# Performance work log

Hardware: AMD Instinct MI355X
Metric: run time of the kernel (lower is better)

The kernel has to match this reference:

```python
import jax, jax.numpy as jnp
import numpy as np

N_NODES = 100000
FEATURES, HIDDEN, CLASSES = 256, 128, 32
N_EDGES = 1600000


def setup_inputs() -> dict:
    key = jax.random.key(0)
    k1, k2, k3, k4, k5 = jax.random.split(key, 5)
    x = jax.random.normal(k1, (N_NODES, FEATURES), dtype=jnp.float32)
    edge_index = jax.random.randint(k2, (2, N_EDGES), 0, N_NODES, dtype=jnp.int64)
    # GCNConv: Linear(in, out, bias=False) + separate bias added after aggregation
    s1 = 1.0 / np.sqrt(FEATURES)
    s2 = 1.0 / np.sqrt(HIDDEN)
    W1 = jax.random.uniform(k3, (FEATURES, HIDDEN), jnp.float32, -s1, s1)
    b1 = jnp.zeros((HIDDEN,), jnp.float32)
    W2 = jax.random.uniform(k4, (HIDDEN, CLASSES), jnp.float32, -s2, s2)
    b2 = jnp.zeros((CLASSES,), jnp.float32)
    return {"x": x, "W1": W1, "b1": b1, "W2": W2, "b2": b2, "edge_index": edge_index}


def _gcn_conv(x, edge_index, W, b, n_nodes):
    # PyG GCNConv with add_self_loops=False: out = D^{-1/2} A D^{-1/2} (X W) + b
    src, dst = edge_index[0], edge_index[1]
    h = x @ W  # [N, out]
    deg = jax.ops.segment_sum(jnp.ones_like(dst, dtype=h.dtype), dst, num_segments=n_nodes)
    dinv = jnp.where(deg > 0, jax.lax.rsqrt(jnp.maximum(deg, 1e-12)), 0.0)
    norm = dinv[src] * dinv[dst]  # [E]
    msgs = h[src] * norm[:, None]  # [E, out] gather + scale
    out = jax.ops.segment_sum(msgs, dst, num_segments=n_nodes)  # scatter-add
    return out + b


def reference(x, W1, b1, W2, b2, edge_index):
    h = _gcn_conv(x, edge_index, W1, b1, N_NODES)
    h = jax.nn.relu(h)
    # F.dropout(training=self.training): eval mode -> identity
    h = _gcn_conv(h, edge_index, W2, b2, N_NODES)
    return jax.nn.log_softmax(h, axis=1)
```

## Files before the change

### kernel.cpp

```cpp
#include <hip/hip_runtime.h>

typedef unsigned short u16;
typedef unsigned int   u32;
typedef __attribute__((ext_vector_type(8))) short short8;
typedef __attribute__((ext_vector_type(4))) float f32x4;
typedef __attribute__((ext_vector_type(2))) float f32x2;

constexpr int BSH = 9;
constexpr int BSZ = 1 << BSH;

__device__ inline float bf2f(u32 bits16) {
    union { u32 u; float f; } c; c.u = bits16 << 16; return c.f;
}
__device__ inline u16 f2bf(float f) {
    union { float f; u32 u; } c; c.f = f;
    return (u16)((c.u + 0x8000u) >> 16);
}
__device__ inline f32x2 up2(u32 h) {
    union { u32 u[2]; f32x2 f; } c;
    c.u[0] = h << 16;
    c.u[1] = h & 0xffff0000u;
    return c.f;
}
__device__ inline int ld_edge(const void* eb, int f64, size_t idx) {
    return f64 ? (int)((const long long*)eb)[idx] : ((const int*)eb)[idx];
}
__device__ inline void gl16(const void* g, void* l) {
    __builtin_amdgcn_global_load_lds(
        (const __attribute__((address_space(1))) unsigned int*)g,
        (__attribute__((address_space(3))) unsigned int*)l, 16, 0, 0);
}

__global__ void detect_kernel(const u32* xw, const int* ebuf_int, int* flags,
                              int* bucket_rsv, int nb, int CAP) {
    __shared__ int cnt;
    if (threadIdx.x == 0) cnt = 0;
    __syncthreads();
    u32 w = xw[threadIdx.x];
    int e = (int)((w >> 7) & 0xffu);
    if (e >= 110 && e <= 145) atomicAdd(&cnt, 1);
    int ev = ebuf_int[2 * threadIdx.x + 1];
    unsigned long long any = __ballot(ev != 0);
    if ((int)threadIdx.x < nb) bucket_rsv[threadIdx.x] = threadIdx.x * CAP;
    __syncthreads();
    if (threadIdx.x == 0) {
        flags[0] = (cnt < 192) ? 1 : 0;
        flags[1] = 0;
        flags[2] = (any == 0ULL) ? 1 : 0;
    }
}

__global__ void bconv_kernel(const void* b1, const void* b2, const int* flags,
                             float* b1f, float* b2f, int HID, int CLS) {
    int i = blockIdx.x * 256 + threadIdx.x;
    int f = flags[0];
    if (i < HID) b1f[i] = f ? ((const float*)b1)[i] : bf2f(((const u16*)b1)[i]);
    if (i < CLS) b2f[i] = f ? ((const float*)b2)[i] : bf2f(((const u16*)b2)[i]);
}

__global__ __launch_bounds__(256)
void passA_kernel(const void* eb, const int* flags, int* bucket_rsv,
                  int2* bpair, int E, int nb, int CAP) {
    __shared__ int hist[256];
    __shared__ int rbase[256];
    hist[threadIdx.x] = 0;
    __syncthreads();
    int f64 = flags[2];
    int base = blockIdx.x * 8192;
    #pragma unroll
    for (int k = 0; k < 32; ++k) {
        int e = base + k * 256 + threadIdx.x;
        if (e < E) {
            int d = ld_edge(eb, f64, (size_t)E + e);
            atomicAdd(&hist[d >> BSH], 1);
        }
    }
    __syncthreads();
    {
        int b = threadIdx.x;
        int c = (b < nb) ? hist[b] : 0;
        rbase[b] = c ? atomicAdd(&bucket_rsv[b], c) : 0;
        hist[b] = 0;
    }
    __syncthreads();
    #pragma unroll
    for (int k = 0; k < 32; ++k) {
        int e = base + k * 256 + threadIdx.x;
        if (e < E) {
            int d = ld_edge(eb, f64, (size_t)E + e);
            int s = ld_edge(eb, f64, (size_t)e);
            int bb = d >> BSH;
            int r = atomicAdd(&hist[bb], 1);
            int pos = rbase[bb] + r;
            if (pos < (bb + 1) * CAP)
                bpair[pos] = make_int2(s, d);
        }
    }
}

__global__ void fillscan_kernel(const int* bucket_rsv, int* bucket_base,
                                int* row_start, int nb, int E, int N, int CAP) {
    __shared__ int wsum[4];
    int t = threadIdx.x, lane = t & 63, wv = t >> 6;
    int v = (t < nb) ? (bucket_rsv[t] - t * CAP) : 0;
    int inc = v;
    #pragma unroll
    for (int d = 1; d < 64; d <<= 1) {
        int tmp = __shfl_up(inc, d, 64);
        if (lane >= d) inc += tmp;
    }
    if (lane == 63) wsum[wv] = inc;
    __syncthreads();
    int off = 0;
    #pragma unroll
    for (int w = 0; w < 4; ++w) if (w < wv) off += wsum[w];
    int excl = off + inc - v;
    if (t <= nb) bucket_base[t] = (t == nb) ? E : excl;
    if (t == 0) row_start[N] = E;
}

__global__ __launch_bounds__(256)
void bucketF_kernel(const int2* __restrict__ bpair, const int* __restrict__ bucket_rsv,
                    const int* __restrict__ bucket_base, float* __restrict__ dinv,
                    int* __restrict__ row_start, int* __restrict__ csr, int N, int CAP) {
    __shared__ int lcnt[BSZ];
    __shared__ int lrow[BSZ];
    __shared__ int wsum[4];
    int b = blockIdx.x, d0 = b << BSH;
    int t = threadIdx.x, lane = t & 63, wv = t >> 6;
    lcnt[2 * t] = 0; lcnt[2 * t + 1] = 0;
    __syncthreads();
    int e0 = b * CAP;
    int e1 = bucket_rsv[b];
    for (int e = e0 + t; e < e1; e += 256)
        atomicAdd(&lcnt[bpair[e].y - d0], 1);
    __syncthreads();
    int c0 = lcnt[2 * t], c1 = lcnt[2 * t + 1];
    int p = c0 + c1;
    int inc = p;
    #pragma unroll
    for (int d = 1; d < 64; d <<= 1) {
        int tmp = __shfl_up(inc, d, 64);
        if (lane >= d) inc += tmp;
    }
    if (lane == 63) wsum[wv] = inc;
    __syncthreads();
    int off = 0;
    #pragma unroll
    for (int w = 0; w < 4; ++w) if (w < wv) off += wsum[w];
    int ex0 = off + inc - p;
    int bb = bucket_base[b];
    lrow[2 * t] = ex0;
    lrow[2 * t + 1] = ex0 + c0;
    int da = d0 + 2 * t, db = d0 + 2 * t + 1;
    if (da < N) { row_start[da] = bb + ex0;      dinv[da] = c0 ? rsqrtf((float)c0) : 0.f; }
    if (db < N) { row_start[db] = bb + ex0 + c0; dinv[db] = c1 ? rsqrtf((float)c1) : 0.f; }
    lcnt[2 * t] = 0; lcnt[2 * t + 1] = 0;
    __syncthreads();
    for (int e = e0 + t; e < e1; e += 256) {
        int2 pr = bpair[e];
        int li = pr.y - d0;
        int r = atomicAdd(&lcnt[li], 1);
        csr[bb + lrow[li] + r] = pr.x;
    }
}

template<int NT, int KT, int NCOLS>
__global__ void prepack_kernel(const void* W, const int* flags, u16* pack) {
    int p = blockIdx.x * 256 + threadIdx.x;
    constexpr int TOT = NT * KT * 64 * 8;
    if (p >= TOT) return;
    int j = p & 7, lane = (p >> 3) & 63, fk = p >> 9;
    int kk = fk % KT, nt = fk / KT;
    int n = nt * 16 + (lane & 15);
    int k = kk * 32 + (lane >> 4) * 8 + j;
    u16 v = flags[0] ? f2bf(((const float*)W)[k * NCOLS + n])
                     : ((const u16*)W)[k * NCOLS + n];
    pack[p] = v;
}

template<int NT, int NTF, int KT, int G>
__global__ __launch_bounds__(256)
void gemm1_kernel(const void* __restrict__ A, const int* __restrict__ ff,
                  const u16* __restrict__ Bpack, const float* __restrict__ dinv,
                  u16* __restrict__ C, int M) {
    constexpr int K = KT * 32;
    constexpr int Ncols = NTF * 16;
    constexpr int NSPLIT = NTF / NT;
    constexpr int BBYTES = NT * KT * 64 * 16;
    __shared__ short8 ldsB[NT * KT * 64];

    const int bh = blockIdx.x % NSPLIT;
    const int bm = blockIdx.x / NSPLIT;
    const int t = threadIdx.x;
    const int wave = t >> 6, lane = t & 63;

    {
        const char* gB = (const char*)Bpack + (size_t)bh * BBYTES;
        char* lB = (char*)ldsB;
        #pragma unroll
        for (int c = 0; c < BBYTES / 4096; ++c)
            gl16(gB + c * 4096 + t * 16, lB + c * 4096 + t * 16);
    }
    const bool fA = (*ff != 0);
    const int m0 = (bm * 4 + wave) * (16 * G);
    const int q = lane >> 4, l16 = lane & 15;

    int rowc[G];
    #pragma unroll
    for (int g = 0; g < G; ++g) {
        int r = m0 + g * 16 + l16;
        rowc[g] = (r < M) ? r : (M - 1);
    }

    f32x4 acc[G][NT];
    #pragma unroll
    for (int g = 0; g < G; ++g)
        #pragma unroll
        for (int nt = 0; nt < NT; ++nt) acc[g][nt] = (f32x4){0.f, 0.f, 0.f, 0.f};

    f32x4 raw[3][G][2];
    const float* Ap[G];
    if (fA) {
        #pragma unroll
        for (int g = 0; g < G; ++g)
            Ap[g] = (const float*)A + (size_t)rowc[g] * K + q * 8;
        #pragma unroll
        for (int pj = 0; pj < 2; ++pj)
            #pragma unroll
            for (int g = 0; g < G; ++g) {
                const float* p = Ap[g] + pj * 32;
                raw[pj][g][0] = ((const f32x4*)p)[0];
                raw[pj][g][1] = ((const f32x4*)p)[1];
            }
        __builtin_amdgcn_sched_barrier(0);
    }
    __syncthreads();

    if (fA) {
        #pragma unroll
        for (int kk = 0; kk < KT; ++kk) {
            if (kk + 2 < KT) {
                #pragma unroll
                for (int g = 0; g < G; ++g) {
                    const float* p = Ap[g] + (kk + 2) * 32;
                    raw[(kk + 2) % 3][g][0] = ((const f32x4*)p)[0];
                    raw[(kk + 2) % 3][g][1] = ((const f32x4*)p)[1];
                }
            }
            __builtin_amdgcn_sched_barrier(0);
            short8 a[G];
            #pragma unroll
            for (int g = 0; g < G; ++g) {
                f32x4 v0 = raw[kk % 3][g][0];
                f32x4 v1 = raw[kk % 3][g][1];
                union { short8 s; u16 u[8]; } pa;
                pa.u[0] = f2bf(v0[0]); pa.u[1] = f2bf(v0[1]);
                pa.u[2] = f2bf(v0[2]); pa.u[3] = f2bf(v0[3]);
                pa.u[4] = f2bf(v1[0]); pa.u[5] = f2bf(v1[1]);
                pa.u[6] = f2bf(v1[2]); pa.u[7] = f2bf(v1[3]);
                a[g] = pa.s;
            }
            #pragma unroll
            for (int nt = 0; nt < NT; ++nt) {
                short8 b = ldsB[(nt * KT + kk) * 64 + lane];
                #pragma unroll
                for (int g = 0; g < G; ++g)
                    acc[g][nt] = __builtin_amdgcn_mfma_f32_16x16x32_bf16(a[g], b, acc[g][nt], 0, 0, 0);
            }
        }
    } else {
        #pragma unroll
        for (int kk = 0; kk < KT; ++kk) {
            short8 a[G];
            #pragma unroll
            for (int g = 0; g < G; ++g)
                a[g] = ((const short8*)((const u16*)A + (size_t)rowc[g] * K))[kk * 4 + q];
            #pragma unroll
            for (int nt = 0; nt < NT; ++nt) {
                short8 b = ldsB[(nt * KT + kk) * 64 + lane];
                #pragma unroll
                for (int g = 0; g < G; ++g)
                    acc[g][nt] = __builtin_amdgcn_mfma_f32_16x16x32_bf16(a[g], b, acc[g][nt], 0, 0, 0);
            }
        }
    }

    #pragma unroll
    for (int g = 0; g < G; ++g) {
        float sc[4];
        #pragma unroll
        for (int r = 0; r < 4; ++r) {
            int rr = m0 + g * 16 + q * 4 + r;
            sc[r] = dinv[(rr < M) ? rr : (M - 1)];
        }
        #pragma unroll
        for (int nt = 0; nt < NT; ++nt) {
            int col = bh * (NT * 16) + nt * 16 + l16;
            #pragma unroll
            for (int r = 0; r < 4; ++r) {
                int rrow = m0 + g * 16 + q * 4 + r;
                if (rrow < M)
                    C[(size_t)rrow * Ncols + col] = f2bf(acc[g][nt][r] * sc[r]);
            }
        }
    }
}

template<int NT, int KT, int G>
__global__ __launch_bounds__(256)
void gemm_kernel(const void* __restrict__ A, const int* __restrict__ ff,
                 const u16* __restrict__ Bpack, const float* __restrict__ dinv,
                 u16* __restrict__ C, int M) {
    constexpr int K = KT * 32;
    constexpr int Ncols = NT * 16;
    __shared__ short8 lds[NT * KT * 64];
    for (int i = threadIdx.x; i < NT * KT * 64; i += 256)
        lds[i] = ((const short8*)Bpack)[i];
    bool fA = (*ff != 0);
    __syncthreads();
    int wave = threadIdx.x >> 6, lane = threadIdx.x & 63;
    int m0 = (blockIdx.x * 4 + wave) * (16 * G);
    if (m0 >= M) return;
    int q = lane >> 4;
    int rowc[G];
    #pragma unroll
    for (int g = 0; g < G; ++g) {
        int r = m0 + g * 16 + (lane & 15);
        rowc[g] = (r < M) ? r : (M - 1);
    }
    f32x4 acc[G][NT];
    #pragma unroll
    for (int g = 0; g < G; ++g)
        #pragma unroll
        for (int nt = 0; nt < NT; ++nt) acc[g][nt] = (f32x4){0.f, 0.f, 0.f, 0.f};
    #pragma unroll
    for (int kk = 0; kk < KT; ++kk) {
        short8 a[G];
        #pragma unroll
        for (int g = 0; g < G; ++g) {
            if (fA) {
                const float* Af = (const float*)A + (size_t)rowc[g] * K + kk * 32 + q * 8;
                f32x4 v0 = ((const f32x4*)Af)[0];
                f32x4 v1 = ((const f32x4*)Af)[1];
                union { short8 s; u16 u[8]; } pa;
                pa.u[0] = f2bf(v0[0]); pa.u[1] = f2bf(v0[1]);
                pa.u[2] = f2bf(v0[2]); pa.u[3] = f2bf(v0[3]);
                pa.u[4] = f2bf(v1[0]); pa.u[5] = f2bf(v1[1]);
                pa.u[6] = f2bf(v1[2]); pa.u[7] = f2bf(v1[3]);
                a[g] = pa.s;
            } else {
                a[g] = ((const short8*)((const u16*)A + (size_t)rowc[g] * K))[kk * 4 + q];
            }
        }
        #pragma unroll
        for (int nt = 0; nt < NT; ++nt) {
            short8 b = lds[(nt * KT + kk) * 64 + lane];
            #pragma unroll
            for (int g = 0; g < G; ++g)
                acc[g][nt] = __builtin_amdgcn_mfma_f32_16x16x32_bf16(a[g], b, acc[g][nt], 0, 0, 0);
        }
    }
    #pragma unroll
    for (int g = 0; g < G; ++g) {
        float sc[4];
        #pragma unroll
        for (int r = 0; r < 4; ++r) {
            int rr = m0 + g * 16 + q * 4 + r;
            sc[r] = dinv[(rr < M) ? rr : (M - 1)];
        }
        #pragma unroll
        for (int nt = 0; nt < NT; ++nt) {
            int col = nt * 16 + (lane & 15);
            #pragma unroll
            for (int r = 0; r < 4; ++r) {
                int rrow = m0 + g * 16 + q * 4 + r;
                if (rrow < M)
                    C[(size_t)rrow * Ncols + col] = f2bf(acc[g][nt][r] * sc[r]);
            }
        }
    }
}

__global__ __launch_bounds__(256)
void agg1_kernel(const u32* __restrict__ H32, const int* __restrict__ csr,
                 const int* __restrict__ row_start, const float* __restrict__ dinv,
                 const float* __restrict__ b1f, u32* __restrict__ H1, int N) {
    int wave = threadIdx.x >> 6, lane = threadIdx.x & 63;
    int n = blockIdx.x * 4 + wave;
    if (n >= N) return;
    int s0 = row_start[n], s1 = row_start[n + 1];
    f32x2 acc = {0.f, 0.f};
    for (int base = s0; base < s1; base += 64) {
        int m = s1 - base; if (m > 64) m = 64;
        int myidx = (lane < m) ? csr[base + lane] : 0;
        int j = 0;
        for (; j + 8 <= m; j += 8) {
            int i0 = __shfl(myidx, j);
            int i1 = __shfl(myidx, j + 1);
            int i2 = __shfl(myidx, j + 2);
            int i3 = __shfl(myidx, j + 3);
            int i4 = __shfl(myidx, j + 4);
            int i5 = __shfl(myidx, j + 5);
            int i6 = __shfl(myidx, j + 6);
            int i7 = __shfl(myidx, j + 7);
            u32 h0 = H32[(size_t)i0 * 64 + lane];
            u32 h1 = H32[(size_t)i1 * 64 + lane];
            u32 h2 = H32[(size_t)i2 * 64 + lane];
            u32 h3 = H32[(size_t)i3 * 64 + lane];
            u32 h4 = H32[(size_t)i4 * 64 + lane];
            u32 h5 = H32[(size_t)i5 * 64 + lane];
            u32 h6 = H32[(size_t)i6 * 64 + lane];
            u32 h7 = H32[(size_t)i7 * 64 + lane];
            f32x2 t0 = up2(h0) + up2(h1);
            f32x2 t1 = up2(h2) + up2(h3);
            f32x2 t2 = up2(h4) + up2(h5);
            f32x2 t3 = up2(h6) + up2(h7);
            acc += (t0 + t1) + (t2 + t3);
        }
        for (; j + 4 <= m; j += 4) {
            int i0 = __shfl(myidx, j);
            int i1 = __shfl(myidx, j + 1);
            int i2 = __shfl(myidx, j + 2);
            int i3 = __shfl(myidx, j + 3);
            u32 h0 = H32[(size_t)i0 * 64 + lane];
            u32 h1 = H32[(size_t)i1 * 64 + lane];
            u32 h2 = H32[(size_t)i2 * 64 + lane];
            u32 h3 = H32[(size_t)i3 * 64 + lane];
            acc += (up2(h0) + up2(h1)) + (up2(h2) + up2(h3));
        }
        for (; j < m; ++j) {
            int s = __shfl(myidx, j);
            acc += up2(H32[(size_t)s * 64 + lane]);
        }
    }
    float wn = dinv[n];
    float v0 = fmaxf(wn * acc.x + b1f[2 * lane], 0.f);
    float v1 = fmaxf(wn * acc.y + b1f[2 * lane + 1], 0.f);
    H1[(size_t)n * 64 + lane] = (u32)f2bf(v0) | ((u32)f2bf(v1) << 16);
}

__global__ __launch_bounds__(256)
void agg2_kernel(const u32* __restrict__ H2, const int* __restrict__ csr,
                 const int* __restrict__ row_start, const float* __restrict__ dinv,
                 const float* __restrict__ b2f, const int* __restrict__ ff,
                 void* __restrict__ out, int N) {
    int wave = threadIdx.x >> 6, lane = threadIdx.x & 63;
    int n = blockIdx.x * 4 + wave;
    if (n >= N) return;
    int l16 = lane & 15, grp = lane >> 4;
    int s0 = row_start[n], s1 = row_start[n + 1];
    f32x2 acc = {0.f, 0.f};
    for (int base = s0; base < s1; base += 64) {
        int m = s1 - base; if (m > 64) m = 64;
        int myidx = (lane < m) ? csr[base + lane] : 0;
        int j = 0;
        for (; j + 8 <= m; j += 8) {
            int ia = __shfl(myidx, j + grp);
            int ib = __shfl(myidx, j + 4 + grp);
            u32 ha = H2[(size_t)ia * 16 + l16];
            u32 hb = H2[(size_t)ib * 16 + l16];
            acc += up2(ha) + up2(hb);
        }
        for (; j < m; j += 4) {
            int jj = j + grp;
            int iv = __shfl(myidx, (jj < m) ? jj : 0);
            if (jj < m) acc += up2(H2[(size_t)iv * 16 + l16]);
        }
    }
    acc.x += __shfl_xor(acc.x, 16); acc.y += __shfl_xor(acc.y, 16);
    acc.x += __shfl_xor(acc.x, 32); acc.y += __shfl_xor(acc.y, 32);
    float wn = dinv[n];
    f32x2 tot;
    tot.x = wn * acc.x + b2f[2 * l16];
    tot.y = wn * acc.y + b2f[2 * l16 + 1];
    float mx = fmaxf(tot.x, tot.y);
    #pragma unroll
    for (int msk = 8; msk; msk >>= 1) mx = fmaxf(mx, __shfl_xor(mx, msk));
    float ex = expf(tot.x - mx) + expf(tot.y - mx);
    #pragma unroll
    for (int msk = 8; msk; msk >>= 1) ex += __shfl_xor(ex, msk);
    float ls = mx + logf(ex);
    if (grp == 0) {
        if (*ff) {
            f32x2 r; r.x = tot.x - ls; r.y = tot.y - ls;
            ((f32x2*)out)[(size_t)n * 16 + l16] = r;
        } else {
            ((u32*)out)[(size_t)n * 16 + l16] =
                (u32)f2bf(tot.x - ls) | ((u32)f2bf(tot.y - ls) << 16);
        }
    }
}

extern "C" void kernel_launch(void* const* d_in, const int* in_sizes, int n_in,
                              void* d_out, int out_size, void* d_ws, size_t ws_size,
                              hipStream_t stream) {
    const void* x  = d_in[0];
    const void* W1 = d_in[1];
    const void* b1 = d_in[2];
    const void* W2 = d_in[3];
    const void* b2 = d_in[4];
    const void* eb = d_in[5];

    const int HID  = in_sizes[2];
    const int CLS  = in_sizes[4];
    const int FEAT = in_sizes[1] / HID;
    const int N    = in_sizes[0] / FEAT;
    const int E    = in_sizes[5] / 2;
    const int nb   = (N + BSZ - 1) >> BSH;
    const int CAP  = (((4 * (E / nb)) >> 10) + 2) << 10;
    (void)n_in; (void)out_size;

    char* w = (char*)d_ws;
    size_t p = 0;
    auto alloc = [&](size_t bytes) {
        size_t o = p; p = (p + bytes + 255) & ~(size_t)255; return o;
    };
    int*   flags      = (int*)  (w + alloc(32));
    int*   row_start  = (int*)  (w + alloc((size_t)(N + 1) * 4));
    int*   bucket_base= (int*)  (w + alloc(257 * 4));
    int*   bucket_rsv = (int*)  (w + alloc(256 * 4));
    int2*  bpair      = (int2*) (w + alloc((size_t)nb * CAP * 8));
    int*   csr        = (int*)  (w + alloc((size_t)E * 4));
    float* dinv       = (float*)(w + alloc((size_t)N * 4));
    float* b1f        = (float*)(w + alloc((size_t)HID * 4));
    float* b2f        = (float*)(w + alloc((size_t)CLS * 4));
    u16*   B1p        = (u16*)  (w + alloc((size_t)FEAT * HID * 2));
    u16*   B2p        = (u16*)  (w + alloc((size_t)HID * CLS * 2));
    u16*   H          = (u16*)  (w + alloc((size_t)N * HID * 2));
    u16*   H1         = (u16*)  (w + alloc((size_t)N * HID * 2));
    u16*   H2         = (u16*)  (w + alloc((size_t)N * CLS * 2));
    if (p > ws_size) return;

    detect_kernel<<<1, 256, 0, stream>>>((const u32*)x, (const int*)eb, flags,
                                         bucket_rsv, nb, CAP);
    bconv_kernel<<<1, 256, 0, stream>>>(b1, b2, flags, b1f, b2f, HID, CLS);

    passA_kernel<<<(E + 8191) / 8192, 256, 0, stream>>>(eb, flags, bucket_rsv,
                                                        bpair, E, nb, CAP);
    fillscan_kernel<<<1, 256, 0, stream>>>(bucket_rsv, bucket_base, row_start,
                                           nb, E, N, CAP);
    bucketF_kernel<<<nb, 256, 0, stream>>>(bpair, bucket_rsv, bucket_base,
                                           dinv, row_start, csr, N, CAP);

    prepack_kernel<8, 8, 128><<<(8 * 8 * 64 * 8 + 255) / 256, 256, 0, stream>>>(W1, flags, B1p);
    prepack_kernel<2, 4, 32><<<(2 * 4 * 64 * 8 + 255) / 256, 256, 0, stream>>>(W2, flags, B2p);

    gemm1_kernel<4, 8, 8, 2><<<2 * ((N + 127) / 128), 256, 0, stream>>>(x, flags, B1p, dinv, H, N);
    agg1_kernel<<<(N + 3) / 4, 256, 0, stream>>>((const u32*)H, csr, row_start, dinv, b1f,
                                                 (u32*)H1, N);
    gemm_kernel<2, 4, 2><<<(N + 127) / 128, 256, 0, stream>>>(H1, flags + 1, B2p, dinv, H2, N);
    agg2_kernel<<<(N + 3) / 4, 256, 0, stream>>>((const u32*)H2, csr, row_start, dinv, b2f,
                                                 flags, (void*)d_out, N);
}
```

Measured before the change: 369.8 us.

## Fuse layer-1 aggregation with second GEMM via shared-memory tile

Merges the first-layer gather/aggregate kernel and the second small GEMM into one kernel. Each 256-thread block aggregates 16 nodes (4 per wave), stages the bf16 hidden rows in LDS, then wave 0 runs MFMA against the prepacked W2 and writes the scaled H2 directly. This removes the H1 intermediate write and read and one kernel launch, at the cost of a block barrier, a serial per-wave node loop, and three idle waves during the MFMA phase.

```diff
diff --git a/kernel.cpp b/kernel.cpp
--- a/kernel.cpp
+++ b/kernel.cpp
@@ -307,137 +307,104 @@
     }
 }
 
-template<int NT, int KT, int G>
 __global__ __launch_bounds__(256)
-void gemm_kernel(const void* __restrict__ A, const int* __restrict__ ff,
-                 const u16* __restrict__ Bpack, const float* __restrict__ dinv,
-                 u16* __restrict__ C, int M) {
-    constexpr int K = KT * 32;
-    constexpr int Ncols = NT * 16;
-    __shared__ short8 lds[NT * KT * 64];
-    for (int i = threadIdx.x; i < NT * KT * 64; i += 256)
-        lds[i] = ((const short8*)Bpack)[i];
-    bool fA = (*ff != 0);
-    __syncthreads();
-    int wave = threadIdx.x >> 6, lane = threadIdx.x & 63;
-    int m0 = (blockIdx.x * 4 + wave) * (16 * G);
-    if (m0 >= M) return;
-    int q = lane >> 4;
-    int rowc[G];
-    #pragma unroll
-    for (int g = 0; g < G; ++g) {
-        int r = m0 + g * 16 + (lane & 15);
-        rowc[g] = (r < M) ? r : (M - 1);
-    }
-    f32x4 acc[G][NT];
-    #pragma unroll
-    for (int g = 0; g < G; ++g)
-        #pragma unroll
-        for (int nt = 0; nt < NT; ++nt) acc[g][nt] = (f32x4){0.f, 0.f, 0.f, 0.f};
-    #pragma unroll
-    for (int kk = 0; kk < KT; ++kk) {
-        short8 a[G];
-        #pragma unroll
-        for (int g = 0; g < G; ++g) {
-            if (fA) {
-                const float* Af = (const float*)A + (size_t)rowc[g] * K + kk * 32 + q * 8;
-                f32x4 v0 = ((const f32x4*)Af)[0];
-                f32x4 v1 = ((const f32x4*)Af)[1];
-                union { short8 s; u16 u[8]; } pa;
-                pa.u[0] = f2bf(v0[0]); pa.u[1] = f2bf(v0[1]);
-                pa.u[2] = f2bf(v0[2]); pa.u[3] = f2bf(v0[3]);
-                pa.u[4] = f2bf(v1[0]); pa.u[5] = f2bf(v1[1]);
-                pa.u[6] = f2bf(v1[2]); pa.u[7] = f2bf(v1[3]);
-                a[g] = pa.s;
-            } else {
-                a[g] = ((const short8*)((const u16*)A + (size_t)rowc[g] * K))[kk * 4 + q];
-            }
-        }
-        #pragma unroll
-        for (int nt = 0; nt < NT; ++nt) {
-            short8 b = lds[(nt * KT + kk) * 64 + lane];
-            #pragma unroll
-            for (int g = 0; g < G; ++g)
-                acc[g][nt] = __builtin_amdgcn_mfma_f32_16x16x32_bf16(a[g], b, acc[g][nt], 0, 0, 0);
-        }
-    }
-    #pragma unroll
-    for (int g = 0; g < G; ++g) {
-        float sc[4];
-        #pragma unroll
-        for (int r = 0; r < 4; ++r) {
-            int rr = m0 + g * 16 + q * 4 + r;
-            sc[r] = dinv[(rr < M) ? rr : (M - 1)];
-        }
-        #pragma unroll
-        for (int nt = 0; nt < NT; ++nt) {
-            int col = nt * 16 + (lane & 15);
+void agg1m_kernel(const u32* __restrict__ H32, const int* __restrict__ csr,
+                  const int* __restrict__ row_start, const float* __restrict__ dinv,
+                  const float* __restrict__ b1f, const u16* __restrict__ B2p,
+                  u16* __restrict__ H2, int N) {
+    __shared__ u32 lh[16][68];
+    __shared__ short8 ldsw[2 * 4 * 64];
+    const int t = threadIdx.x;
+    const int wave = t >> 6, lane = t & 63;
+    ldsw[t]       = ((const short8*)B2p)[t];
+    ldsw[t + 256] = ((const short8*)B2p)[t + 256];
+    const int nb = blockIdx.x * 16;
+    #pragma unroll 1
+    for (int u = 0; u < 4; ++u) {
+        int n = nb + wave * 4 + u;
+        u32 packed = 0;
+        if (n < N) {
+            int s0 = row_start[n], s1 = row_start[n + 1];
+            f32x2 acc = {0.f, 0.f};
+            for (int base = s0; base < s1; base += 64) {
+                int m = s1 - base; if (m > 64) m = 64;
+                int myidx = (lane < m) ? csr[base + lane] : 0;
+                int j = 0;
+                for (; j + 8 <= m; j += 8) {
+                    int i0 = __shfl(myidx, j);
+                    int i1 = __shfl(myidx, j + 1);
+                    int i2 = __shfl(myidx, j + 2);
+                    int i3 = __shfl(myidx, j + 3);
+                    int i4 = __shfl(myidx, j + 4);
+                    int i5 = __shfl(myidx, j + 5);
+                    int i6 = __shfl(myidx, j + 6);
+                    int i7 = __shfl(myidx, j + 7);
+                    u32 h0 = H32[(size_t)i0 * 64 + lane];
+                    u32 h1 = H32[(size_t)i1 * 64 + lane];
+                    u32 h2 = H32[(size_t)i2 * 64 + lane];
+                    u32 h3 = H32[(size_t)i3 * 64 + lane];
+                    u32 h4 = H32[(size_t)i4 * 64 + lane];
+                    u32 h5 = H32[(size_t)i5 * 64 + lane];
+                    u32 h6 = H32[(size_t)i6 * 64 + lane];
+                    u32 h7 = H32[(size_t)i7 * 64 + lane];
+                    f32x2 t0 = up2(h0) + up2(h1);
+                    f32x2 t1 = up2(h2) + up2(h3);
+                    f32x2 t2 = up2(h4) + up2(h5);
+                    f32x2 t3 = up2(h6) + up2(h7);
+                    acc += (t0 + t1) + (t2 + t3);
+                }
+                for (; j + 4 <= m; j += 4) {
+                    int i0 = __shfl(myidx, j);
+                    int i1 = __shfl(myidx, j + 1);
+                    int i2 = __shfl(myidx, j + 2);
+                    int i3 = __shfl(myidx, j + 3);
+                    u32 h0 = H32[(size_t)i0 * 64 + lane];
+                    u32 h1 = H32[(size_t)i1 * 64 + lane];
+                    u32 h2 = H32[(size_t)i2 * 64 + lane];
+                    u32 h3 = H32[(size_t)i3 * 64 + lane];
+                    acc += (up2(h0) + up2(h1)) + (up2(h2) + up2(h3));
+                }
+                for (; j < m; ++j) {
+                    int s = __shfl(myidx, j);
+                    acc += up2(H32[(size_t)s * 64 + lane]);
+                }
+            }
+            float wn = dinv[n];
+            float v0 = fmaxf(wn * acc.x + b1f[2 * lane], 0.f);
+            float v1 = fmaxf(wn * acc.y + b1f[2 * lane + 1], 0.f);
+            packed = (u32)f2bf(v0) | ((u32)f2bf(v1) << 16);
+        }
+        lh[wave * 4 + u][lane] = packed;
+    }
+    __syncthreads();
+    if (wave == 0) {
+        const int q = lane >> 4, l16 = lane & 15;
+        f32x4 acc2[2];
+        acc2[0] = (f32x4){0.f, 0.f, 0.f, 0.f};
+        acc2[1] = (f32x4){0.f, 0.f, 0.f, 0.f};
+        #pragma unroll
+        for (int kk = 0; kk < 4; ++kk) {
+            short8 a = *(const short8*)&lh[l16][kk * 16 + q * 4];
+            #pragma unroll
+            for (int nt = 0; nt < 2; ++nt) {
+                short8 b = ldsw[(nt * 4 + kk) * 64 + lane];
+                acc2[nt] = __builtin_amdgcn_mfma_f32_16x16x32_bf16(a, b, acc2[nt], 0, 0, 0);
+            }
+        }
+        #pragma unroll
+        for (int nt = 0; nt < 2; ++nt) {
+            int col = nt * 16 + l16;
             #pragma unroll
             for (int r = 0; r < 4; ++r) {
-                int rrow = m0 + g * 16 + q * 4 + r;
-                if (rrow < M)
-                    C[(size_t)rrow * Ncols + col] = f2bf(acc[g][nt][r] * sc[r]);
-            }
-        }
-    }
-}
-
-__global__ __launch_bounds__(256)
-void agg1_kernel(const u32* __restrict__ H32, const int* __restrict__ csr,
-                 const int* __restrict__ row_start, const float* __restrict__ dinv,
-                 const float* __restrict__ b1f, u32* __restrict__ H1, int N) {
-    int wave = threadIdx.x >> 6, lane = threadIdx.x & 63;
-    int n = blockIdx.x * 4 + wave;
-    if (n >= N) return;
-    int s0 = row_start[n], s1 = row_start[n + 1];
-    f32x2 acc = {0.f, 0.f};
-    for (int base = s0; base < s1; base += 64) {
-        int m = s1 - base; if (m > 64) m = 64;
-        int myidx = (lane < m) ? csr[base + lane] : 0;
-        int j = 0;
-        for (; j + 8 <= m; j += 8) {
-            int i0 = __shfl(myidx, j);
-            int i1 = __shfl(myidx, j + 1);
-            int i2 = __shfl(myidx, j + 2);
-            int i3 = __shfl(myidx, j + 3);
-            int i4 = __shfl(myidx, j + 4);
-            int i5 = __shfl(myidx, j + 5);
-            int i6 = __shfl(myidx, j + 6);
-            int i7 = __shfl(myidx, j + 7);
-            u32 h0 = H32[(size_t)i0 * 64 + lane];
-            u32 h1 = H32[(size_t)i1 * 64 + lane];
-            u32 h2 = H32[(size_t)i2 * 64 + lane];
-            u32 h3 = H32[(size_t)i3 * 64 + lane];
-            u32 h4 = H32[(size_t)i4 * 64 + lane];
-            u32 h5 = H32[(size_t)i5 * 64 + lane];
-            u32 h6 = H32[(size_t)i6 * 64 + lane];
-            u32 h7 = H32[(size_t)i7 * 64 + lane];
-            f32x2 t0 = up2(h0) + up2(h1);
-            f32x2 t1 = up2(h2) + up2(h3);
-            f32x2 t2 = up2(h4) + up2(h5);
-            f32x2 t3 = up2(h6) + up2(h7);
-            acc += (t0 + t1) + (t2 + t3);
-        }
-        for (; j + 4 <= m; j += 4) {
-            int i0 = __shfl(myidx, j);
-            int i1 = __shfl(myidx, j + 1);
-            int i2 = __shfl(myidx, j + 2);
-            int i3 = __shfl(myidx, j + 3);
-            u32 h0 = H32[(size_t)i0 * 64 + lane];
-            u32 h1 = H32[(size_t)i1 * 64 + lane];
-            u32 h2 = H32[(size_t)i2 * 64 + lane];
-            u32 h3 = H32[(size_t)i3 * 64 + lane];
-            acc += (up2(h0) + up2(h1)) + (up2(h2) + up2(h3));
-        }
-        for (; j < m; ++j) {
-            int s = __shfl(myidx, j);
-            acc += up2(H32[(size_t)s * 64 + lane]);
-        }
-    }
-    float wn = dinv[n];
-    float v0 = fmaxf(wn * acc.x + b1f[2 * lane], 0.f);
-    float v1 = fmaxf(wn * acc.y + b1f[2 * lane + 1], 0.f);
-    H1[(size_t)n * 64 + lane] = (u32)f2bf(v0) | ((u32)f2bf(v1) << 16);
+                int row = q * 4 + r;
+                int rn = nb + row;
+                if (rn < N) {
+                    float sc = dinv[rn];
+                    H2[(size_t)rn * 32 + col] = f2bf(acc2[nt][r] * sc);
+                }
+            }
+        }
+    }
 }
 
 __global__ __launch_bounds__(256)
@@ -528,7 +495,6 @@
     u16*   B1p        = (u16*)  (w + alloc((size_t)FEAT * HID * 2));
     u16*   B2p        = (u16*)  (w + alloc((size_t)HID * CLS * 2));
     u16*   H          = (u16*)  (w + alloc((size_t)N * HID * 2));
-    u16*   H1         = (u16*)  (w + alloc((size_t)N * HID * 2));
     u16*   H2         = (u16*)  (w + alloc((size_t)N * CLS * 2));
     if (p > ws_size) return;
 
@@ -547,9 +513,8 @@
     prepack_kernel<2, 4, 32><<<(2 * 4 * 64 * 8 + 255) / 256, 256, 0, stream>>>(W2, flags, B2p);
 
     gemm1_kernel<4, 8, 8, 2><<<2 * ((N + 127) / 128), 256, 0, stream>>>(x, flags, B1p, dinv, H, N);
-    agg1_kernel<<<(N + 3) / 4, 256, 0, stream>>>((const u32*)H, csr, row_start, dinv, b1f,
-                                                 (u32*)H1, N);
-    gemm_kernel<2, 4, 2><<<(N + 127) / 128, 256, 0, stream>>>(H1, flags + 1, B2p, dinv, H2, N);
+    agg1m_kernel<<<(N + 15) / 16, 256, 0, stream>>>((const u32*)H, csr, row_start, dinv,
+                                                    b1f, B2p, H2, N);
     agg2_kernel<<<(N + 3) / 4, 256, 0, stream>>>((const u32*)H2, csr, row_start, dinv, b2f,
                                                  flags, (void*)d_out, N);
 }
```

Measured after the change: 363.7 us. About the same (-1.6%).
